# Optimization experiments

Measured on AMD Instinct MI355X. Metric: run time of the kernel, lower is better.

Reference implementation:

```python
import jax, jax.numpy as jnp
import numpy as np

HEADS = 8
DIM_HEAD = 32
DIM = 256           # must equal HEADS*DIM_HEAD (required by the torch view)
HIDDEN = HEADS * DIM_HEAD
NUM_GROUPS = 32
EPS = 1e-6


def setup_inputs() -> dict:
    key = jax.random.key(0)
    ks = jax.random.split(key, 6)
    b, c, h, w = 16, DIM, 64, 64
    x = jax.random.normal(ks[0], (b, c, h, w), dtype=jnp.float32)
    # conv1x1 weights stored as 2D matrices (out_ch, in_ch)
    w_qkv = jax.random.normal(ks[1], (3 * HIDDEN, DIM), dtype=jnp.float32) * (1.0 / np.sqrt(DIM))
    w_out = jax.random.normal(ks[2], (DIM, HIDDEN), dtype=jnp.float32) * (1.0 / np.sqrt(HIDDEN))
    b_out = jax.random.normal(ks[3], (DIM,), dtype=jnp.float32) * 0.01
    gn_gamma = jnp.ones((DIM,), dtype=jnp.float32)
    gn_beta = jnp.zeros((DIM,), dtype=jnp.float32)
    return {"x": x, "w_qkv": w_qkv, "w_out": w_out, "b_out": b_out,
            "gn_gamma": gn_gamma, "gn_beta": gn_beta}


def _group_norm(x, gamma, beta):
    # GroupNorm32: compute in float32, eps=1e-6, affine
    b, c, h, w = x.shape
    g = NUM_GROUPS
    xf = x.astype(jnp.float32).reshape(b, g, c // g, h, w)
    mean = xf.mean(axis=(2, 3, 4), keepdims=True)
    var = xf.var(axis=(2, 3, 4), keepdims=True)
    xn = (xf - mean) * jax.lax.rsqrt(var + EPS)
    xn = xn.reshape(b, c, h, w)
    return (xn * gamma[None, :, None, None] + beta[None, :, None, None]).astype(x.dtype)


def reference(x, w_qkv, w_out, b_out, gn_gamma, gn_beta):
    b, c, h, w = x.shape
    n = h * w
    # qkv projection (1x1 conv == matmul over channels)
    qkv = jnp.einsum('oc,bchw->bohw', w_qkv, x)            # (b, 3*hidden, h, w)
    qkv = qkv.reshape(b, 3, HEADS, DIM_HEAD, n)
    q, k, v = qkv[:, 0], qkv[:, 1], qkv[:, 2]              # (b, h, d, n)
    q = jax.nn.softmax(q, axis=-2)                         # softmax over feature dim
    k = jax.nn.softmax(k, axis=-1)                         # softmax over spatial dim
    context = jnp.einsum('bhdn,bhen->bhde', k, v)          # (b, heads, d, d)
    out = jnp.einsum('bhde,bhdn->bhen', context, q)        # (b, heads, d, n)
    out = out.reshape(b, c, h, w)
    out = jnp.einsum('oc,bchw->bohw', w_out, out) + b_out[None, :, None, None]
    out = _group_norm(out, gn_gamma, gn_beta)
    return out + x
```

## Files before the change

kernel.cpp:

```cpp
#include <hip/hip_runtime.h>


typedef short s8v __attribute__((ext_vector_type(8)));
typedef float f32x4 __attribute__((ext_vector_type(4)));

__device__ __forceinline__ short f2bf(float f) {
  union { float f; unsigned u; } v; v.f = f;
  unsigned r = v.u + 0x7FFF + ((v.u >> 16) & 1);
  return (short)(r >> 16);
}
__device__ __forceinline__ float bf2f(short h) {
  union { unsigned u; float f; } v; v.u = ((unsigned)(unsigned short)h) << 16;
  return v.f;
}
__device__ __forceinline__ void gld16(const short* g, short* l) {
  __builtin_amdgcn_global_load_lds(
      (const __attribute__((address_space(1))) unsigned*)g,
      (__attribute__((address_space(3))) unsigned*)l, 16, 0, 0);
}

__global__ __launch_bounds__(256) void cast_to_bf16(
    const float* __restrict__ src, short* __restrict__ dst, int n8) {
  int id = blockIdx.x * 256 + threadIdx.x;
  if (id >= n8) return;
  long off = (long)id * 8;
  float4 a = *(const float4*)&src[off];
  float4 b = *(const float4*)&src[off + 4];
  s8v o;
  o[0] = f2bf(a.x); o[1] = f2bf(a.y); o[2] = f2bf(a.z); o[3] = f2bf(a.w);
  o[4] = f2bf(b.x); o[5] = f2bf(b.y); o[6] = f2bf(b.z); o[7] = f2bf(b.w);
  *(s8v*)&dst[off] = o;
}

__global__ __launch_bounds__(256) void zero_stats(float* __restrict__ p) {
  p[blockIdx.x * 256 + threadIdx.x] = 0.f;
}

__global__ __launch_bounds__(256) void cast_transpose_x(
    const float* __restrict__ x, short* __restrict__ xt) {
  int b = blockIdx.z;
  int n0 = blockIdx.x * 64, c0 = blockIdx.y * 64;
  __shared__ short ls[64][65];
  int t = threadIdx.x;
  const float* xb = x + ((long)b * 256 + c0) * 4096 + n0;
  int ci = t >> 4, j4 = (t & 15) * 4;
#pragma unroll
  for (int i = 0; i < 4; ++i) {
    int cl = ci + i * 16;
    float4 v = *(const float4*)&xb[(long)cl * 4096 + j4];
    ls[j4 + 0][cl] = f2bf(v.x);
    ls[j4 + 1][cl] = f2bf(v.y);
    ls[j4 + 2][cl] = f2bf(v.z);
    ls[j4 + 3][cl] = f2bf(v.w);
  }
  __syncthreads();
  short* xtb = xt + ((long)b * 4096 + n0) * 256 + c0;
#pragma unroll
  for (int i = 0; i < 2; ++i) {
    int id = t + i * 256;
    int nl = id >> 3, c8 = (id & 7) * 8;
    s8v o;
#pragma unroll
    for (int e = 0; e < 8; ++e) o[e] = ls[nl][c8 + e];
    *(s8v*)&xtb[(long)nl * 256 + c8] = o;
  }
}

__global__ __launch_bounds__(256) void gemm_qkv(
    const short* __restrict__ A, const short* __restrict__ Bt,
    short* __restrict__ kv, short* __restrict__ qT) {
  __shared__ short lA[2][8192];
  __shared__ short lB[2][8192];
  int b = blockIdx.z;
  int mt = blockIdx.y * 128, nt = blockIdx.x * 128;
  int tid = threadIdx.x;
  int lane = tid & 63;
  int wm = tid >> 7, wn = (tid >> 6) & 1;
  int rl = lane & 15, kg = lane >> 4;
  const short* Ab = A + (long)mt * 256;
  const short* Bb = Bt + ((long)b * 4096 + nt) * 256;

  f32x4 acc[4][4];
#pragma unroll
  for (int i = 0; i < 4; ++i)
#pragma unroll
    for (int j = 0; j < 4; ++j) acc[i][j] = (f32x4){0.f, 0.f, 0.f, 0.f};

  auto stage = [&](int buf, int k0) {
#pragma unroll
    for (int is = 0; is < 4; ++is) {
      int s = is * 256 + tid;
      int row = s >> 3, kcp = s & 7;
      int kcl = kcp ^ (row & 7);
      gld16(Ab + (long)row * 256 + k0 + kcl * 8, &lA[buf][(is * 256 + (tid & ~63)) * 8]);
      gld16(Bb + (long)row * 256 + k0 + kcl * 8, &lB[buf][(is * 256 + (tid & ~63)) * 8]);
    }
  };

  stage(0, 0);
#pragma unroll
  for (int s = 0; s < 4; ++s) {
    int cur = s & 1;
    if (s < 3) {
      stage(cur ^ 1, (s + 1) * 64);
      asm volatile("s_waitcnt vmcnt(8)" ::: "memory");
    } else {
      asm volatile("s_waitcnt vmcnt(0)" ::: "memory");
    }
    __builtin_amdgcn_s_barrier();
#pragma unroll
    for (int kw = 0; kw < 2; ++kw) {
      int kc = kw * 4 + kg;
      s8v av[4], bv[4];
#pragma unroll
      for (int mi = 0; mi < 4; ++mi) {
        int row = wm * 64 + mi * 16 + rl;
        av[mi] = *(const s8v*)&lA[cur][row * 64 + ((kc ^ (row & 7)) << 3)];
      }
#pragma unroll
      for (int ni = 0; ni < 4; ++ni) {
        int row = wn * 64 + ni * 16 + rl;
        bv[ni] = *(const s8v*)&lB[cur][row * 64 + ((kc ^ (row & 7)) << 3)];
      }
#pragma unroll
      for (int mi = 0; mi < 4; ++mi)
#pragma unroll
        for (int ni = 0; ni < 4; ++ni)
          acc[mi][ni] = __builtin_amdgcn_mfma_f32_16x16x32_bf16(
              av[mi], bv[ni], acc[mi][ni], 0, 0, 0);
    }
    asm volatile("s_waitcnt lgkmcnt(0)" ::: "memory");
    __builtin_amdgcn_s_barrier();
  }

  if (mt < 256) {
    short* qTb = qT + ((long)b * 4096 + nt) * 256 + mt;
#pragma unroll
    for (int ni = 0; ni < 4; ++ni) {
      int n = wn * 64 + ni * 16 + rl;
#pragma unroll
      for (int p = 0; p < 2; ++p) {
        float v[8];
        float m = -1e30f;
#pragma unroll
        for (int j = 0; j < 8; ++j) {
          v[j] = acc[p * 2 + (j >> 2)][ni][j & 3];
          m = fmaxf(m, v[j]);
        }
        m = fmaxf(m, __shfl_xor(m, 16));
        m = fmaxf(m, __shfl_xor(m, 32));
        float ssum = 0.f;
#pragma unroll
        for (int j = 0; j < 8; ++j) { v[j] = __expf(v[j] - m); ssum += v[j]; }
        ssum += __shfl_xor(ssum, 16);
        ssum += __shfl_xor(ssum, 32);
        float inv = 1.f / ssum;
#pragma unroll
        for (int half = 0; half < 2; ++half) {
          short4 o;
          o.x = f2bf(v[half * 4 + 0] * inv);
          o.y = f2bf(v[half * 4 + 1] * inv);
          o.z = f2bf(v[half * 4 + 2] * inv);
          o.w = f2bf(v[half * 4 + 3] * inv);
          *(short4*)&qTb[(long)n * 256 + wm * 64 + p * 32 + half * 16 + kg * 4] = o;
        }
      }
    }
  } else {
    short* Cb = kv + ((long)b * 512 + (mt - 256)) * 4096 + nt;
#pragma unroll
    for (int mi = 0; mi < 4; ++mi) {
#pragma unroll
      for (int r = 0; r < 4; ++r) {
        int o = wm * 64 + mi * 16 + kg * 4 + r;
#pragma unroll
        for (int ni = 0; ni < 4; ++ni) {
          int n = wn * 64 + ni * 16 + rl;
          Cb[(long)o * 4096 + n] = f2bf(acc[mi][ni][r]);
        }
      }
    }
  }
}

__global__ __launch_bounds__(256) void gemm_lin(
    const short* __restrict__ A, const short* __restrict__ Bt,
    short* __restrict__ C, const float* __restrict__ bias,
    float* __restrict__ st2) {
  __shared__ short lA[2][8192];
  __shared__ short lB[2][8192];
  int b = blockIdx.z;
  int mt = blockIdx.y * 128, nt = blockIdx.x * 128;
  int tid = threadIdx.x;
  int lane = tid & 63;
  int wm = tid >> 7, wn = (tid >> 6) & 1;
  int rl = lane & 15, kg = lane >> 4;
  const short* Ab = A + (long)b * 65536 + (long)mt * 256;
  const short* Bb = Bt + ((long)b * 4096 + nt) * 256;

  f32x4 acc[4][4];
#pragma unroll
  for (int i = 0; i < 4; ++i)
#pragma unroll
    for (int j = 0; j < 4; ++j) acc[i][j] = (f32x4){0.f, 0.f, 0.f, 0.f};

  auto stage = [&](int buf, int k0) {
#pragma unroll
    for (int is = 0; is < 4; ++is) {
      int s = is * 256 + tid;
      int row = s >> 3, kcp = s & 7;
      int kcl = kcp ^ (row & 7);
      gld16(Ab + (long)row * 256 + k0 + kcl * 8, &lA[buf][(is * 256 + (tid & ~63)) * 8]);
      gld16(Bb + (long)row * 256 + k0 + kcl * 8, &lB[buf][(is * 256 + (tid & ~63)) * 8]);
    }
  };

  stage(0, 0);
#pragma unroll
  for (int s = 0; s < 4; ++s) {
    int cur = s & 1;
    if (s < 3) {
      stage(cur ^ 1, (s + 1) * 64);
      asm volatile("s_waitcnt vmcnt(8)" ::: "memory");
    } else {
      asm volatile("s_waitcnt vmcnt(0)" ::: "memory");
    }
    __builtin_amdgcn_s_barrier();
#pragma unroll
    for (int kw = 0; kw < 2; ++kw) {
      int kc = kw * 4 + kg;
      s8v av[4], bv[4];
#pragma unroll
      for (int mi = 0; mi < 4; ++mi) {
        int row = wm * 64 + mi * 16 + rl;
        av[mi] = *(const s8v*)&lA[cur][row * 64 + ((kc ^ (row & 7)) << 3)];
      }
#pragma unroll
      for (int ni = 0; ni < 4; ++ni) {
        int row = wn * 64 + ni * 16 + rl;
        bv[ni] = *(const s8v*)&lB[cur][row * 64 + ((kc ^ (row & 7)) << 3)];
      }
#pragma unroll
      for (int mi = 0; mi < 4; ++mi)
#pragma unroll
        for (int ni = 0; ni < 4; ++ni)
          acc[mi][ni] = __builtin_amdgcn_mfma_f32_16x16x32_bf16(
              av[mi], bv[ni], acc[mi][ni], 0, 0, 0);
    }
    asm volatile("s_waitcnt lgkmcnt(0)" ::: "memory");
    __builtin_amdgcn_s_barrier();
  }

  short* Cb = C + ((long)b * 256 + mt) * 4096 + nt;
  float s1[4] = {0.f, 0.f, 0.f, 0.f};
  float s2[4] = {0.f, 0.f, 0.f, 0.f};
#pragma unroll
  for (int mi = 0; mi < 4; ++mi) {
#pragma unroll
    for (int r = 0; r < 4; ++r) {
      int o = wm * 64 + mi * 16 + kg * 4 + r;
      float bv = bias[mt + o];
#pragma unroll
      for (int ni = 0; ni < 4; ++ni) {
        int n = wn * 64 + ni * 16 + rl;
        short h = f2bf(acc[mi][ni][r] + bv);
        Cb[(long)o * 4096 + n] = h;
        float q = bf2f(h);
        s1[mi] += q;
        s2[mi] += q * q;
      }
    }
  }
#pragma unroll
  for (int mi = 0; mi < 4; ++mi) {
#pragma unroll
    for (int off = 1; off <= 16; off <<= 1) {
      s1[mi] += __shfl_xor(s1[mi], off);
      s2[mi] += __shfl_xor(s2[mi], off);
    }
    if (rl == 0 && (kg & 1) == 0) {
      int g = (mt >> 3) + wm * 8 + mi * 2 + (kg >> 1);
      atomicAdd(&st2[(b * 32 + g) * 2], s1[mi]);
      atomicAdd(&st2[(b * 32 + g) * 2 + 1], s2[mi]);
    }
  }
}

__global__ __launch_bounds__(256) void ctx_mfma(
    const short* __restrict__ kv, float* __restrict__ ctxp, float* __restrict__ sp) {
  int split = blockIdx.x;
  int h = blockIdx.y, b = blockIdx.z;
  int tid = threadIdx.x;
  int w = tid >> 6, l = tid & 63;
  const short* kb = kv + ((long)(b * 512) + h * 32) * 4096;
  const short* vb = kb + (long)256 * 4096;
  int rl = l & 15, kg = l >> 4;
  int n_base = split * 1024 + w * 256;

  f32x4 acc[2][2];
#pragma unroll
  for (int i = 0; i < 2; ++i)
#pragma unroll
    for (int j = 0; j < 2; ++j) acc[i][j] = (f32x4){0.f, 0.f, 0.f, 0.f};
  float s_part0 = 0.f, s_part1 = 0.f;

#pragma unroll 2
  for (int it = 0; it < 8; ++it) {
    int n0 = n_base + it * 32 + kg * 8;
    s8v a0, a1, b0, b1;
    {
      s8v kr = *(const s8v*)&kb[(long)rl * 4096 + n0];
#pragma unroll
      for (int j = 0; j < 8; ++j) {
        float f = __expf(bf2f(kr[j]));
        s_part0 += f;
        a0[j] = f2bf(f);
      }
    }
    {
      s8v kr = *(const s8v*)&kb[(long)(16 + rl) * 4096 + n0];
#pragma unroll
      for (int j = 0; j < 8; ++j) {
        float f = __expf(bf2f(kr[j]));
        s_part1 += f;
        a1[j] = f2bf(f);
      }
    }
    b0 = *(const s8v*)&vb[(long)rl * 4096 + n0];
    b1 = *(const s8v*)&vb[(long)(16 + rl) * 4096 + n0];
    acc[0][0] = __builtin_amdgcn_mfma_f32_16x16x32_bf16(a0, b0, acc[0][0], 0, 0, 0);
    acc[0][1] = __builtin_amdgcn_mfma_f32_16x16x32_bf16(a0, b1, acc[0][1], 0, 0, 0);
    acc[1][0] = __builtin_amdgcn_mfma_f32_16x16x32_bf16(a1, b0, acc[1][0], 0, 0, 0);
    acc[1][1] = __builtin_amdgcn_mfma_f32_16x16x32_bf16(a1, b1, acc[1][1], 0, 0, 0);
  }
  s_part0 += __shfl_xor(s_part0, 16); s_part0 += __shfl_xor(s_part0, 32);
  s_part1 += __shfl_xor(s_part1, 16); s_part1 += __shfl_xor(s_part1, 32);

  __shared__ float lctx[4][1024];
  __shared__ float lsum[4][32];
#pragma unroll
  for (int di = 0; di < 2; ++di)
#pragma unroll
    for (int ei = 0; ei < 2; ++ei)
#pragma unroll
      for (int r = 0; r < 4; ++r) {
        int row = di * 16 + kg * 4 + r;
        int col = ei * 16 + rl;
        lctx[w][row * 32 + col] = acc[di][ei][r];
      }
  if (kg == 0) { lsum[w][rl] = s_part0; lsum[w][16 + rl] = s_part1; }
  __syncthreads();
  long base = (long)(b * 8 + h) * 4 + split;
#pragma unroll
  for (int i = 0; i < 4; ++i) {
    int id = tid + i * 256;
    ctxp[base * 1024 + id] = lctx[0][id] + lctx[1][id] + lctx[2][id] + lctx[3][id];
  }
  if (tid < 32)
    sp[base * 32 + tid] = lsum[0][tid] + lsum[1][tid] + lsum[2][tid] + lsum[3][tid];
}

__global__ __launch_bounds__(256) void make_wf(
    const float* __restrict__ ctxp, const float* __restrict__ sp,
    const float* __restrict__ w_out, short* __restrict__ wf) {
  int h = blockIdx.x, b = blockIdx.y;
  __shared__ float c[32][33];
  __shared__ float inv_s[32];
  __shared__ float wv[256][33];
  int t = threadIdx.x;
  long base = (long)(b * 8 + h) * 4;
#pragma unroll
  for (int i = 0; i < 4; ++i) {
    int id = t + i * 256;
    float v = ctxp[base * 1024 + id] + ctxp[(base + 1) * 1024 + id] +
              ctxp[(base + 2) * 1024 + id] + ctxp[(base + 3) * 1024 + id];
    c[id >> 5][id & 31] = v;
  }
  if (t < 32) {
    float sv = sp[base * 32 + t] + sp[(base + 1) * 32 + t] +
               sp[(base + 2) * 32 + t] + sp[(base + 3) * 32 + t];
    inv_s[t] = 1.f / sv;
  }
#pragma unroll
  for (int r = 0; r < 32; ++r) {
    int row = r * 8 + (t >> 5);
    wv[row][t & 31] = w_out[row * 256 + h * 32 + (t & 31)];
  }
  __syncthreads();
  float wr[32];
#pragma unroll
  for (int e = 0; e < 32; ++e) wr[e] = wv[t][e];
  float tmp[32];
#pragma unroll
  for (int dd = 0; dd < 32; ++dd) {
    float sum = 0.f;
#pragma unroll
    for (int e = 0; e < 32; ++e) sum += wr[e] * c[dd][e];
    tmp[dd] = sum * inv_s[dd];
  }
  short* dst = wf + ((long)b * 256 + t) * 256 + h * 32;
#pragma unroll
  for (int c8 = 0; c8 < 4; ++c8) {
    s8v o;
#pragma unroll
    for (int e = 0; e < 8; ++e) o[e] = f2bf(tmp[c8 * 8 + e]);
    *(s8v*)&dst[c8 * 8] = o;
  }
}

__global__ __launch_bounds__(256) void final_out(
    const short* __restrict__ lin, const float* __restrict__ x,
    const float2* __restrict__ st2, const float* __restrict__ gamma,
    const float* __restrict__ beta, float* __restrict__ out) {
  long id = (long)blockIdx.x * 256 + threadIdx.x;
  long e0 = id * 8;
  int b = (int)(e0 >> 20);
  int rem = (int)(e0 & 1048575);
  int c = rem >> 12;
  float2 st = st2[b * 32 + (c >> 3)];
  float mean = st.x * (1.f / 32768.f);
  float inv = rsqrtf(st.y * (1.f / 32768.f) - mean * mean + 1e-6f);
  float ga = gamma[c] * inv;
  float be = beta[c] - mean * ga;
  s8v l8 = *(const s8v*)&lin[e0];
  float4 x0 = *(const float4*)&x[e0];
  float4 x1 = *(const float4*)&x[e0 + 4];
  float4 o0, o1;
  o0.x = bf2f(l8[0]) * ga + be + x0.x;
  o0.y = bf2f(l8[1]) * ga + be + x0.y;
  o0.z = bf2f(l8[2]) * ga + be + x0.z;
  o0.w = bf2f(l8[3]) * ga + be + x0.w;
  o1.x = bf2f(l8[4]) * ga + be + x1.x;
  o1.y = bf2f(l8[5]) * ga + be + x1.y;
  o1.z = bf2f(l8[6]) * ga + be + x1.z;
  o1.w = bf2f(l8[7]) * ga + be + x1.w;
  *(float4*)&out[e0] = o0;
  *(float4*)&out[e0 + 4] = o1;
}

extern "C" void kernel_launch(void* const* d_in, const int* in_sizes, int n_in,
                              void* d_out, int out_size, void* d_ws, size_t ws_size,
                              hipStream_t stream) {
  const float* x     = (const float*)d_in[0];
  const float* w_qkv = (const float*)d_in[1];
  const float* w_out = (const float*)d_in[2];
  const float* b_out = (const float*)d_in[3];
  const float* gamma = (const float*)d_in[4];
  const float* beta  = (const float*)d_in[5];
  float* out = (float*)d_out;

  short* xt   = (short*)d_ws;
  short* qT   = xt + 16777216;
  short* kvb  = qT + 16777216;
  short* lin  = kvb + 33554432;
  short* wqb  = lin + 16777216;
  short* wfb  = wqb + 196608;
  float* ctxp = (float*)(wfb + 1048576);
  float* sp   = ctxp + 524288;
  float* st2  = sp + 16384;

  cast_to_bf16<<<96, 256, 0, stream>>>(w_qkv, wqb, 24576);
  zero_stats<<<4, 256, 0, stream>>>(st2);
  cast_transpose_x<<<dim3(64, 4, 16), 256, 0, stream>>>(x, xt);
  gemm_qkv<<<dim3(32, 6, 16), 256, 0, stream>>>(wqb, xt, kvb, qT);
  ctx_mfma<<<dim3(4, 8, 16), 256, 0, stream>>>(kvb, ctxp, sp);
  make_wf<<<dim3(8, 16), 256, 0, stream>>>(ctxp, sp, w_out, wfb);
  gemm_lin<<<dim3(32, 2, 16), 256, 0, stream>>>(wfb, qT, lin, b_out, st2);
  final_out<<<8192, 256, 0, stream>>>(lin, x, (const float2*)st2, gamma, beta, out);
}
```

Measured before the change: 161.9 us.

## Load GEMM A-operand directly to registers and merge weight cast with stats zeroing

Both GEMM kernels stop staging the small, cache-resident A operand (weights) through LDS and instead load it straight from global memory into registers each k-step. This halves the LDS footprint and the LDS traffic, which may allow higher occupancy. The waitcnt is adjusted to match the reduced number of async loads. The weight-cast and stats-zeroing kernels are merged into one launch to save a kernel dispatch. The risk is extra global/L2 load latency exposed at the start of each k-step, since the register loads are issued right before use.

```diff
diff --git a/kernel.cpp b/kernel.cpp
--- a/kernel.cpp
+++ b/kernel.cpp
@@ -19,10 +19,14 @@
       (__attribute__((address_space(3))) unsigned*)l, 16, 0, 0);
 }
 
-__global__ __launch_bounds__(256) void cast_to_bf16(
-    const float* __restrict__ src, short* __restrict__ dst, int n8) {
+__global__ __launch_bounds__(256) void cast_w(
+    const float* __restrict__ src, short* __restrict__ dst, float* __restrict__ st2) {
+  if (blockIdx.x == 96) {
+    float4 z = {0.f, 0.f, 0.f, 0.f};
+    ((float4*)st2)[threadIdx.x] = z;
+    return;
+  }
   int id = blockIdx.x * 256 + threadIdx.x;
-  if (id >= n8) return;
   long off = (long)id * 8;
   float4 a = *(const float4*)&src[off];
   float4 b = *(const float4*)&src[off + 4];
@@ -30,10 +34,6 @@
   o[0] = f2bf(a.x); o[1] = f2bf(a.y); o[2] = f2bf(a.z); o[3] = f2bf(a.w);
   o[4] = f2bf(b.x); o[5] = f2bf(b.y); o[6] = f2bf(b.z); o[7] = f2bf(b.w);
   *(s8v*)&dst[off] = o;
-}
-
-__global__ __launch_bounds__(256) void zero_stats(float* __restrict__ p) {
-  p[blockIdx.x * 256 + threadIdx.x] = 0.f;
 }
 
 __global__ __launch_bounds__(256) void cast_transpose_x(
@@ -69,7 +69,6 @@
 __global__ __launch_bounds__(256) void gemm_qkv(
     const short* __restrict__ A, const short* __restrict__ Bt,
     short* __restrict__ kv, short* __restrict__ qT) {
-  __shared__ short lA[2][8192];
   __shared__ short lB[2][8192];
   int b = blockIdx.z;
   int mt = blockIdx.y * 128, nt = blockIdx.x * 128;
@@ -92,7 +91,6 @@
       int s = is * 256 + tid;
       int row = s >> 3, kcp = s & 7;
       int kcl = kcp ^ (row & 7);
-      gld16(Ab + (long)row * 256 + k0 + kcl * 8, &lA[buf][(is * 256 + (tid & ~63)) * 8]);
       gld16(Bb + (long)row * 256 + k0 + kcl * 8, &lB[buf][(is * 256 + (tid & ~63)) * 8]);
     }
   };
@@ -101,9 +99,18 @@
 #pragma unroll
   for (int s = 0; s < 4; ++s) {
     int cur = s & 1;
+    int k0 = s * 64;
+    s8v av[2][4];
+#pragma unroll
+    for (int kw = 0; kw < 2; ++kw)
+#pragma unroll
+      for (int mi = 0; mi < 4; ++mi) {
+        int row = wm * 64 + mi * 16 + rl;
+        av[kw][mi] = *(const s8v*)&Ab[(long)row * 256 + k0 + (kw * 4 + kg) * 8];
+      }
     if (s < 3) {
-      stage(cur ^ 1, (s + 1) * 64);
-      asm volatile("s_waitcnt vmcnt(8)" ::: "memory");
+      stage(cur ^ 1, k0 + 64);
+      asm volatile("s_waitcnt vmcnt(4)" ::: "memory");
     } else {
       asm volatile("s_waitcnt vmcnt(0)" ::: "memory");
     }
@@ -111,12 +118,7 @@
 #pragma unroll
     for (int kw = 0; kw < 2; ++kw) {
       int kc = kw * 4 + kg;
-      s8v av[4], bv[4];
-#pragma unroll
-      for (int mi = 0; mi < 4; ++mi) {
-        int row = wm * 64 + mi * 16 + rl;
-        av[mi] = *(const s8v*)&lA[cur][row * 64 + ((kc ^ (row & 7)) << 3)];
-      }
+      s8v bv[4];
 #pragma unroll
       for (int ni = 0; ni < 4; ++ni) {
         int row = wn * 64 + ni * 16 + rl;
@@ -127,7 +129,7 @@
 #pragma unroll
         for (int ni = 0; ni < 4; ++ni)
           acc[mi][ni] = __builtin_amdgcn_mfma_f32_16x16x32_bf16(
-              av[mi], bv[ni], acc[mi][ni], 0, 0, 0);
+              av[kw][mi], bv[ni], acc[mi][ni], 0, 0, 0);
     }
     asm volatile("s_waitcnt lgkmcnt(0)" ::: "memory");
     __builtin_amdgcn_s_barrier();
@@ -187,7 +189,6 @@
     const short* __restrict__ A, const short* __restrict__ Bt,
     short* __restrict__ C, const float* __restrict__ bias,
     float* __restrict__ st2) {
-  __shared__ short lA[2][8192];
   __shared__ short lB[2][8192];
   int b = blockIdx.z;
   int mt = blockIdx.y * 128, nt = blockIdx.x * 128;
@@ -210,7 +211,6 @@
       int s = is * 256 + tid;
       int row = s >> 3, kcp = s & 7;
       int kcl = kcp ^ (row & 7);
-      gld16(Ab + (long)row * 256 + k0 + kcl * 8, &lA[buf][(is * 256 + (tid & ~63)) * 8]);
       gld16(Bb + (long)row * 256 + k0 + kcl * 8, &lB[buf][(is * 256 + (tid & ~63)) * 8]);
     }
   };
@@ -219,9 +219,18 @@
 #pragma unroll
   for (int s = 0; s < 4; ++s) {
     int cur = s & 1;
+    int k0 = s * 64;
+    s8v av[2][4];
+#pragma unroll
+    for (int kw = 0; kw < 2; ++kw)
+#pragma unroll
+      for (int mi = 0; mi < 4; ++mi) {
+        int row = wm * 64 + mi * 16 + rl;
+        av[kw][mi] = *(const s8v*)&Ab[(long)row * 256 + k0 + (kw * 4 + kg) * 8];
+      }
     if (s < 3) {
-      stage(cur ^ 1, (s + 1) * 64);
-      asm volatile("s_waitcnt vmcnt(8)" ::: "memory");
+      stage(cur ^ 1, k0 + 64);
+      asm volatile("s_waitcnt vmcnt(4)" ::: "memory");
     } else {
       asm volatile("s_waitcnt vmcnt(0)" ::: "memory");
     }
@@ -229,12 +238,7 @@
 #pragma unroll
     for (int kw = 0; kw < 2; ++kw) {
       int kc = kw * 4 + kg;
-      s8v av[4], bv[4];
-#pragma unroll
-      for (int mi = 0; mi < 4; ++mi) {
-        int row = wm * 64 + mi * 16 + rl;
-        av[mi] = *(const s8v*)&lA[cur][row * 64 + ((kc ^ (row & 7)) << 3)];
-      }
+      s8v bv[4];
 #pragma unroll
       for (int ni = 0; ni < 4; ++ni) {
         int row = wn * 64 + ni * 16 + rl;
@@ -245,7 +249,7 @@
 #pragma unroll
         for (int ni = 0; ni < 4; ++ni)
           acc[mi][ni] = __builtin_amdgcn_mfma_f32_16x16x32_bf16(
-              av[mi], bv[ni], acc[mi][ni], 0, 0, 0);
+              av[kw][mi], bv[ni], acc[mi][ni], 0, 0, 0);
     }
     asm volatile("s_waitcnt lgkmcnt(0)" ::: "memory");
     __builtin_amdgcn_s_barrier();
@@ -459,8 +463,7 @@
   float* sp   = ctxp + 524288;
   float* st2  = sp + 16384;
 
-  cast_to_bf16<<<96, 256, 0, stream>>>(w_qkv, wqb, 24576);
-  zero_stats<<<4, 256, 0, stream>>>(st2);
+  cast_w<<<97, 256, 0, stream>>>(w_qkv, wqb, st2);
   cast_transpose_x<<<dim3(64, 4, 16), 256, 0, stream>>>(x, xt);
   gemm_qkv<<<dim3(32, 6, 16), 256, 0, stream>>>(wqb, xt, kvb, qT);
   ctx_mfma<<<dim3(4, 8, 16), 256, 0, stream>>>(kvb, ctxp, sp);
```

After: 182.9 us. 13.0% more time.
